# Kernel optimization log

Hardware: AMD Instinct MI355X
Metric: run time of the kernel (lower is better)

Reference implementation:

```python
import jax, jax.numpy as jnp
import numpy as np

EMB_DIM = 256
ATT_DIM = 256
B, S = 8, 2048


def setup_inputs() -> dict:
    key = jax.random.key(0)
    ks = jax.random.split(key, 9)
    scale = 1.0 / np.sqrt(EMB_DIM)
    inp = {
        "x": jax.random.normal(ks[0], (B, S, EMB_DIM), dtype=jnp.float32),
        "mask": jax.random.randint(ks[1], (B, S, S), 0, 2, dtype=jnp.int32),
        "Wq": jax.random.uniform(ks[2], (EMB_DIM, ATT_DIM), jnp.float32, -scale, scale),
        "bq": jax.random.uniform(ks[3], (ATT_DIM,), jnp.float32, -scale, scale),
        "Wk": jax.random.uniform(ks[4], (EMB_DIM, ATT_DIM), jnp.float32, -scale, scale),
        "bk": jax.random.uniform(ks[5], (ATT_DIM,), jnp.float32, -scale, scale),
        "Wv": jax.random.uniform(ks[6], (EMB_DIM, ATT_DIM), jnp.float32, -scale, scale),
        "bv": jax.random.uniform(ks[7], (ATT_DIM,), jnp.float32, -scale, scale),
    }
    return inp


def reference(x, mask, Wq, bq, Wk, bk, Wv, bv):
    # Linear projections: (B,S,E) @ (E,A) + (A,)
    q = jnp.einsum("bse,ea->bsa", x, Wq) + bq
    k = jnp.einsum("bse,ea->bsa", x, Wk) + bk
    v = jnp.einsum("bse,ea->bsa", x, Wv) + bv
    # scores: (B,S,S)
    scores = jnp.einsum("bqa,bka->bqk", q, k) / jnp.sqrt(jnp.float32(ATT_DIM))
    scores = jnp.where(mask == 0, jnp.float32(-1e9), scores)
    attn = jax.nn.softmax(scores, axis=-1)
    return jnp.einsum("bqk,bka->bqa", attn, v)
```

## Files before the change

### kernel.cpp

```cpp
#include <hip/hip_runtime.h>
#include <hip/hip_bf16.h>
#include <stdint.h>

#define BATCH 8
#define SEQ   2048
#define EMB   256
#define ADIM  256

typedef __bf16 bf16_t;
typedef __attribute__((ext_vector_type(8))) __bf16 bf16x8;
typedef __attribute__((ext_vector_type(4))) float  f32x4;
typedef uint32_t u32;
typedef __attribute__((ext_vector_type(4))) u32 u32x4;
typedef long long i64;

static __device__ __forceinline__ f32x4 mfma16(bf16x8 a, bf16x8 b, f32x4 c) {
    return __builtin_amdgcn_mfma_f32_16x16x32_bf16(a, b, c, 0, 0, 0);
}

static __device__ __forceinline__ void gld16(const void* g, void* l) {
    __builtin_amdgcn_global_load_lds((const __attribute__((address_space(1))) u32*)g,
                                     (__attribute__((address_space(3))) u32*)l, 16, 0, 0);
}

__global__ __launch_bounds__(256) void wtkv_kernel(const float* __restrict__ Wk,
                                                   const float* __restrict__ Wv,
                                                   bf16_t* __restrict__ wt) {
    int tid = blockIdx.x * 256 + threadIdx.x;
    int m = tid >> 16;
    int i = tid & 65535;
    int a = i >> 8, e = i & 255;
    const float* W = (m == 0) ? Wk : Wv;
    wt[m * 65536 + a * 256 + e] = (bf16_t)W[e * 256 + a];
}

__global__ __launch_bounds__(256) void maskbits_kernel(const u32* __restrict__ mask,
                                                       u32* __restrict__ bitw) {
    int idx = blockIdx.x * 256 + threadIdx.x;
    const u32* mp = mask + (size_t)idx * 32;
    u32 wd = 0;
    #pragma unroll
    for (int q = 0; q < 8; ++q) {
        u32x4 v = *(const u32x4*)(mp + q * 4);
        #pragma unroll
        for (int j = 0; j < 4; ++j)
            wd |= (v[j] ? 1u : 0u) << (q * 4 + j);
    }
    bitw[idx] = wd;
}

__global__ __launch_bounds__(128, 1) void proj_kv(const float* __restrict__ x,
                                                  const bf16_t* __restrict__ wt,
                                                  const float* __restrict__ bk,
                                                  const float* __restrict__ bv,
                                                  char* __restrict__ Ksw,
                                                  char* __restrict__ Vsw) {
    __shared__ __align__(16) char stg[2][10240];
    const int tid  = threadIdx.x;
    const int wid  = tid >> 6;
    const int lane = tid & 63;
    const int lq   = lane >> 4;
    const int ln   = lane & 15;
    const int blk  = blockIdx.x;
    const int b    = blk >> 6;
    const int tile = blk & 63;
    const int mbase = blk * 32 + wid * 16;
    char* S = stg[wid];

    bf16x8 xf[8];
    const float* xp = x + (size_t)(mbase + ln) * EMB;
    #pragma unroll
    for (int c = 0; c < 8; ++c) {
        f32x4 a0 = *(const f32x4*)(xp + c * 32 + lq * 8);
        f32x4 a1 = *(const f32x4*)(xp + c * 32 + lq * 8 + 4);
        bf16x8 v;
        v[0] = (bf16_t)a0[0]; v[1] = (bf16_t)a0[1]; v[2] = (bf16_t)a0[2]; v[3] = (bf16_t)a0[3];
        v[4] = (bf16_t)a1[0]; v[5] = (bf16_t)a1[1]; v[6] = (bf16_t)a1[2]; v[7] = (bf16_t)a1[3];
        xf[c] = v;
    }

    f32x4 acc[16];

    #pragma unroll
    for (int t = 0; t < 16; ++t) acc[t] = (f32x4){0.f, 0.f, 0.f, 0.f};
    {
        const bf16_t* w = wt;
        #pragma unroll
        for (int c = 0; c < 8; ++c)
            #pragma unroll
            for (int t = 0; t < 16; ++t) {
                bf16x8 wf = *(const bf16x8*)(w + (size_t)(t * 16 + ln) * 256 + c * 32 + lq * 8);
                acc[t] = mfma16(xf[c], wf, acc[t]);
            }
    }
    #pragma unroll
    for (int t = 0; t < 16; ++t) {
        float bb = bk[t * 16 + ln];
        #pragma unroll
        for (int r = 0; r < 4; ++r)
            *(bf16_t*)(S + (lq * 4 + r) * 512 + (t * 16 + ln) * 2) = (bf16_t)(acc[t][r] + bb);
    }
    asm volatile("s_waitcnt lgkmcnt(0)" ::: "memory");
    {
        char* Kg = Ksw + (size_t)b * 1048576 + (size_t)tile * 16384 + wid * 8192;
        const int rh = lane >> 5;
        const int p  = lane & 31;
        #pragma unroll
        for (int i = 0; i < 8; ++i) {
            int row = i * 2 + rh;
            int n   = wid * 16 + row;
            int cb  = p ^ (n & 7);
            f32x4 ch = *(const f32x4*)(S + row * 512 + cb * 16);
            *(f32x4*)(Kg + row * 512 + p * 16) = ch;
        }
    }

    #pragma unroll
    for (int t = 0; t < 16; ++t) acc[t] = (f32x4){0.f, 0.f, 0.f, 0.f};
    {
        const bf16_t* w = wt + 65536;
        #pragma unroll
        for (int c = 0; c < 8; ++c)
            #pragma unroll
            for (int t = 0; t < 16; ++t) {
                bf16x8 wf = *(const bf16x8*)(w + (size_t)(t * 16 + ln) * 256 + c * 32 + lq * 8);
                acc[t] = mfma16(xf[c], wf, acc[t]);
            }
    }
    #pragma unroll
    for (int t = 0; t < 16; ++t) {
        float bb = bv[t * 16 + ln];
        #pragma unroll
        for (int r = 0; r < 4; ++r)
            *(bf16_t*)(S + (t * 16 + ln) * 40 + (lq * 4 + r) * 2) = (bf16_t)(acc[t][r] + bb);
    }
    asm volatile("s_waitcnt lgkmcnt(0)" ::: "memory");
    {
        char* Vg = Vsw + (size_t)b * 1048576 + (size_t)tile * 16384;
        const int half = lane & 1;
        const int kq   = wid * 2 + half;
        #pragma unroll
        for (int i = 0; i < 8; ++i) {
            int a   = i * 32 + (lane >> 1);
            int pos = kq ^ (a & 3) ^ ((a >> 2) & 3);
            f32x4 ch = *(const f32x4*)(S + a * 40 + half * 16);
            *(f32x4*)(Vg + a * 64 + pos * 16) = ch;
        }
    }
}

__global__ __launch_bounds__(512, 4) void flash_kernel(const float* __restrict__ x,
                                                       const float* __restrict__ WqM,
                                                       const float* __restrict__ bq,
                                                       const char* __restrict__ Ksw,
                                                       const char* __restrict__ Vsw,
                                                       const int* __restrict__ mask,
                                                       const u32* __restrict__ bitw,
                                                       float* __restrict__ lp,
                                                       i64 bs, i64 rs, i64 ks,
                                                       float* __restrict__ out) {
    __shared__ __align__(16) char smem[76288];
    const int tid  = threadIdx.x;
    const int wid  = tid >> 6;
    const int lane = tid & 63;
    const int lq   = lane >> 4;
    const int ln   = lane & 15;
    const int qw   = wid >> 1;
    const int kw   = wid & 1;
    const int batch = blockIdx.x & 7;
    const int kvh   = (blockIdx.x >> 3) & 1;
    const int qbase = (blockIdx.x >> 4) * 64;

    const char* Kb = Ksw + (size_t)batch * 1048576 + (size_t)(kvh * 32) * 16384;
    const char* Vb = Vsw + (size_t)batch * 1048576 + (size_t)(kvh * 32) * 16384;
    char*  Pq_ = smem + 65536 + qw * 1280;
    char*  Pt  = smem + 65536 + wid * 1280;
    float* Ls  = (float*)(smem + 75776);

    const int dhalf = wid >> 2, dqr = wid & 3;
    const char* gsrc0 = (dhalf ? Vb : Kb) + dqr * 4096 + lane * 16;
    const int   ldst0 = dhalf * 16384 + dqr * 4096;

    const int* mroot = mask + (size_t)batch * SEQ * SEQ +
                       (size_t)(qbase + qw * 16) * SEQ + kvh * 1024 + kw * 16 + ln;
    const u32* broot = bitw ? bitw + (size_t)batch * 131072 +
                              (size_t)(qbase + qw * 16) * 64 + kvh * 32
                            : nullptr;
    const int bitpos = kw * 16 + ln;

    {
        char* dl = smem + ldst0;
        #pragma unroll
        for (int i = 0; i < 4; ++i) gld16(gsrc0 + i * 1024, dl + i * 1024);
    }
    asm volatile("" ::: "memory");
    int mv[2][4];
    if (broot) {
        #pragma unroll
        for (int w = 0; w < 2; ++w)
            #pragma unroll
            for (int r = 0; r < 4; ++r)
                mv[w][r] = (int)((broot[(lq * 4 + r) * 64 + w] >> bitpos) & 1u);
    } else {
        #pragma unroll
        for (int w = 0; w < 2; ++w)
            #pragma unroll
            for (int r = 0; r < 4; ++r)
                mv[w][r] = mroot[(size_t)(lq * 4 + r) * SEQ + w * 32];
    }

    bf16x8 qf[8];
    {
        bf16x8 xf[8];
        {
            const float* xp = x + (size_t)(batch * SEQ + qbase + qw * 16 + ln) * EMB;
            #pragma unroll
            for (int c = 0; c < 8; ++c) {
                f32x4 a = *(const f32x4*)(xp + c * 32 + lq * 8);
                f32x4 b = *(const f32x4*)(xp + c * 32 + lq * 8 + 4);
                bf16x8 v;
                v[0] = (bf16_t)a[0]; v[1] = (bf16_t)a[1]; v[2] = (bf16_t)a[2]; v[3] = (bf16_t)a[3];
                v[4] = (bf16_t)b[0]; v[5] = (bf16_t)b[1]; v[6] = (bf16_t)b[2]; v[7] = (bf16_t)b[3];
                xf[c] = v;
            }
        }
        f32x4 qacc[16];
        #pragma unroll
        for (int t = 0; t < 16; ++t) qacc[t] = (f32x4){0.f, 0.f, 0.f, 0.f};

        char* Wsp = smem + 32768;
        const int grp = tid >> 8;
        const int aa  = tid & 255;
        const int e   = ln & 7;
        #pragma unroll 1
        for (int cp = 0; cp < 8; ++cp) {
            __syncthreads();
            const float* wqp = WqM + (size_t)(cp * 32) * 256 + aa;
            #pragma unroll
            for (int i = 0; i < 2; ++i) {
                int ip = grp * 2 + i;
                bf16x8 pk;
                #pragma unroll
                for (int j = 0; j < 8; ++j)
                    pk[j] = (bf16_t)wqp[(size_t)(ip * 8 + j) * 256];
                *(bf16x8*)(Wsp + aa * 128 + ((ip ^ (aa & 7)) * 16)) = pk;
            }
            __syncthreads();
            #pragma unroll
            for (int t = 0; t < 16; ++t) {
                bf16x8 wf = *(const bf16x8*)(Wsp + (t * 16 + ln) * 128 + ((lq ^ e) * 16));
                qacc[t] = mfma16(xf[cp], wf, qacc[t]);
            }
        }
        #pragma unroll
        for (int c = 0; c < 8; ++c) {
            #pragma unroll
            for (int half2 = 0; half2 < 2; ++half2) {
                int t = 2 * c + half2;
                float bb = bq[t * 16 + ln];
                #pragma unroll
                for (int r = 0; r < 4; ++r) {
                    float v = (qacc[t][r] + bb) * 0.0625f;
                    ((bf16_t*)(Pt + (lq * 4 + r) * 80))[half2 * 16 + ln] = (bf16_t)v;
                }
            }
            qf[c] = *(const bf16x8*)(Pt + ln * 80 + lq * 16);
        }
    }

    f32x4 o[8];
    #pragma unroll
    for (int t = 0; t < 8; ++t) o[t] = (f32x4){0.f, 0.f, 0.f, 0.f};
    float lsum[4] = {0.f, 0.f, 0.f, 0.f};

    const int kswz = ln & 7;
    const int vswz = (lq ^ (ln & 3) ^ ((ln >> 2) & 3)) * 16;
    const int n0   = kw * 16 + ln;

    for (int kt = 0; kt < 32; ++kt) {
        asm volatile("s_waitcnt vmcnt(4) lgkmcnt(0)\n\ts_barrier" ::: "memory");
        if (kt + 1 < 32) {
            const char* gs = gsrc0 + (size_t)(kt + 1) * 16384;
            char* dl = smem + ((kt + 1) & 1) * 32768 + ldst0;
            #pragma unroll
            for (int i = 0; i < 4; ++i) gld16(gs + i * 1024, dl + i * 1024);
        }
        const char* Ksb = smem + (kt & 1) * 32768;
        const char* Vsb = Ksb + 16384;

        f32x4 s0 = (f32x4){0.f, 0.f, 0.f, 0.f};
        const char* krow = Ksb + n0 * 512;
        #pragma unroll
        for (int c = 0; c < 8; ++c) {
            bf16x8 kf = *(const bf16x8*)(krow + (((c * 4 + lq) ^ kswz) * 16));
            s0 = mfma16(qf[c], kf, s0);
        }

        const int* mc = mv[kt & 1];
        #pragma unroll
        for (int r = 0; r < 4; ++r) {
            float p0 = mc[r] ? __expf(s0[r]) : 0.f;
            lsum[r] += p0;
            ((bf16_t*)(Pq_ + (lq * 4 + r) * 80))[kw * 16 + ln] = (bf16_t)p0;
        }

        asm volatile("s_waitcnt lgkmcnt(0)\n\ts_barrier" ::: "memory");

        {
            const int ktn = (kt + 2 < 32) ? kt + 2 : 31;
            int* md = mv[kt & 1];
            if (broot) {
                #pragma unroll
                for (int r = 0; r < 4; ++r)
                    md[r] = (int)((broot[(lq * 4 + r) * 64 + ktn] >> bitpos) & 1u);
            } else {
                #pragma unroll
                for (int r = 0; r < 4; ++r)
                    md[r] = mroot[(size_t)(lq * 4 + r) * SEQ + ktn * 32];
            }
        }

        bf16x8 pa0 = *(const bf16x8*)(Pq_ + ln * 80 + lq * 16);

        const char* vbase = Vsb + (kw * 128 + ln) * 64 + vswz;
        #pragma unroll
        for (int t = 0; t < 8; ++t) {
            bf16x8 vf = *(const bf16x8*)(vbase + t * 1024);
            o[t] = mfma16(pa0, vf, o[t]);
        }
    }

    __syncthreads();
    #pragma unroll
    for (int r = 0; r < 4; ++r) {
        float v = lsum[r];
        v += __shfl_xor(v, 1);
        v += __shfl_xor(v, 2);
        v += __shfl_xor(v, 4);
        v += __shfl_xor(v, 8);
        if (ln == 0) Ls[(qw * 2 + kw) * 16 + lq * 4 + r] = v;
        lsum[r] = v;
    }
    __syncthreads();

    if (kw == 0 && ln == 0) {
        #pragma unroll
        for (int r = 0; r < 4; ++r) {
            int row = lq * 4 + r;
            float tot = lsum[r] + Ls[(qw * 2 + 1) * 16 + row];
            lp[bs * batch + rs * (qbase + qw * 16 + row) + ks * kvh] = tot;
        }
    }

    #pragma unroll
    for (int r = 0; r < 4; ++r) {
        float* orow = out + (size_t)(batch * SEQ + qbase + qw * 16 + lq * 4 + r) * ADIM
                      + kw * 128 + ln;
        #pragma unroll
        for (int t = 0; t < 8; ++t)
            atomicAdd(orow + t * 16, o[t][r]);
    }
}

__global__ __launch_bounds__(256) void merge_kernel(const float* __restrict__ lp,
                                                    i64 bs, i64 rs, i64 ks,
                                                    float* __restrict__ out) {
    int idx  = blockIdx.x * 256 + threadIdx.x;
    int base = idx * 4;
    int row  = base >> 8;
    int b = row >> 11, r = row & 2047;
    float l0 = lp[bs * b + rs * r];
    float l1 = lp[bs * b + rs * r + ks];
    float inv = 1.0f / (l0 + l1);
    f32x4 v = *(const f32x4*)(out + base);
    v[0] *= inv; v[1] *= inv; v[2] *= inv; v[3] *= inv;
    *(f32x4*)(out + base) = v;
}

extern "C" void kernel_launch(void* const* d_in, const int* in_sizes, int n_in,
                              void* d_out, int out_size, void* d_ws, size_t ws_size,
                              hipStream_t stream) {
    const float* x    = (const float*)d_in[0];
    int*         mask = (int*)d_in[1];
    const float* Wq   = (const float*)d_in[2];
    const float* bq   = (const float*)d_in[3];
    const float* Wk   = (const float*)d_in[4];
    const float* bk   = (const float*)d_in[5];
    const float* Wv   = (const float*)d_in[6];
    const float* bv   = (const float*)d_in[7];
    float* out = (float*)d_out;

    char* Ksw = (char*)d_ws;
    char* Vsw = Ksw + (size_t)8 * 1024 * 1024;
    bf16_t* wt = (bf16_t*)d_out;

    const size_t MB = 1024 * 1024;
    const size_t lsum_bytes = (size_t)2 * BATCH * SEQ * sizeof(float);
    u32*   bitw = nullptr;
    float* lp; i64 bs, rs, ks;
    if (ws_size >= 20 * MB + lsum_bytes) {
        bitw = (u32*)(Ksw + 16 * MB);
        lp = (float*)(Ksw + 20 * MB);
        bs = (i64)2 * SEQ;  rs = 2;  ks = 1;
    } else if (ws_size >= 16 * MB + lsum_bytes) {
        lp = (float*)(Ksw + 16 * MB);
        bs = (i64)2 * SEQ;  rs = 2;  ks = 1;
    } else {
        lp = (float*)mask;
        bs = (i64)SEQ * SEQ;  rs = SEQ;  ks = 1024;
    }

    wtkv_kernel<<<512, 256, 0, stream>>>(Wk, Wv, wt);
    if (bitw) maskbits_kernel<<<4096, 256, 0, stream>>>((const u32*)mask, bitw);
    proj_kv<<<512, 128, 0, stream>>>(x, wt, bk, bv, Ksw, Vsw);
    hipMemsetAsync(d_out, 0, (size_t)out_size * sizeof(float), stream);
    flash_kernel<<<512, 512, 0, stream>>>(x, Wq, bq, Ksw, Vsw, mask, bitw,
                                          lp, bs, rs, ks, out);
    merge_kernel<<<4096, 256, 0, stream>>>(lp, bs, rs, ks, out);
}
```

Before: 379.5 us.

## Precompute Q projection in projection kernel and simplify flash kernel to 4 waves

Moves the Q projection (with the 1/sqrt(d) scale folded in) out of the flash kernel and into the shared projection kernel, which writes a swizzled bf16 Q buffer to workspace. A new lean flash kernel with 256 threads loads Q fragments from that buffer, double-buffers K/V tiles through LDS, and feeds the bitmask straight into the exp and P-shuffle path. The previous flash kernel is kept as a fallback for when the workspace is too small. The trade is an extra 8MB workspace write and read in exchange for removing the in-kernel fp32 Q projection and reducing LDS and thread count per block. It also assumes a larger workspace is available, and it does not subtract a running max before the exponent, so it depends on scores staying small enough not to overflow.

```diff
diff --git a/kernel.cpp b/kernel.cpp
--- a/kernel.cpp
+++ b/kernel.cpp
@@ -23,14 +23,21 @@
                                      (__attribute__((address_space(3))) u32*)l, 16, 0, 0);
 }
 
+static __device__ __forceinline__ u32 pk2(float lo, float hi) {
+    u32 a = (u32)__builtin_bit_cast(unsigned short, (bf16_t)lo);
+    u32 b = (u32)__builtin_bit_cast(unsigned short, (bf16_t)hi);
+    return a | (b << 16);
+}
+
 __global__ __launch_bounds__(256) void wtkv_kernel(const float* __restrict__ Wk,
                                                    const float* __restrict__ Wv,
+                                                   const float* __restrict__ Wq,
                                                    bf16_t* __restrict__ wt) {
     int tid = blockIdx.x * 256 + threadIdx.x;
     int m = tid >> 16;
     int i = tid & 65535;
     int a = i >> 8, e = i & 255;
-    const float* W = (m == 0) ? Wk : Wv;
+    const float* W = (m == 0) ? Wk : (m == 1) ? Wv : Wq;
     wt[m * 65536 + a * 256 + e] = (bf16_t)W[e * 256 + a];
 }
 
@@ -49,12 +56,14 @@
     bitw[idx] = wd;
 }
 
-__global__ __launch_bounds__(128, 1) void proj_kv(const float* __restrict__ x,
-                                                  const bf16_t* __restrict__ wt,
-                                                  const float* __restrict__ bk,
-                                                  const float* __restrict__ bv,
-                                                  char* __restrict__ Ksw,
-                                                  char* __restrict__ Vsw) {
+__global__ __launch_bounds__(128, 1) void proj_qkv(const float* __restrict__ x,
+                                                   const bf16_t* __restrict__ wt,
+                                                   const float* __restrict__ bk,
+                                                   const float* __restrict__ bv,
+                                                   const float* __restrict__ bq,
+                                                   char* __restrict__ Ksw,
+                                                   char* __restrict__ Vsw,
+                                                   char* __restrict__ Qsw) {
     __shared__ __align__(16) char stg[2][10240];
     const int tid  = threadIdx.x;
     const int wid  = tid >> 6;
@@ -115,6 +124,43 @@
         }
     }
 
+    if (Qsw) {
+        #pragma unroll
+        for (int t = 0; t < 16; ++t) acc[t] = (f32x4){0.f, 0.f, 0.f, 0.f};
+        {
+            const bf16_t* w = wt + 131072;
+            #pragma unroll
+            for (int c = 0; c < 8; ++c)
+                #pragma unroll
+                for (int t = 0; t < 16; ++t) {
+                    bf16x8 wf = *(const bf16x8*)(w + (size_t)(t * 16 + ln) * 256 + c * 32 + lq * 8);
+                    acc[t] = mfma16(xf[c], wf, acc[t]);
+                }
+        }
+        #pragma unroll
+        for (int t = 0; t < 16; ++t) {
+            float bb = bq[t * 16 + ln];
+            #pragma unroll
+            for (int r = 0; r < 4; ++r)
+                *(bf16_t*)(S + (lq * 4 + r) * 512 + (t * 16 + ln) * 2) =
+                    (bf16_t)((acc[t][r] + bb) * 0.0625f);
+        }
+        asm volatile("s_waitcnt lgkmcnt(0)" ::: "memory");
+        {
+            char* Qg = Qsw + (size_t)b * 1048576 + (size_t)tile * 16384 + wid * 8192;
+            const int rh = lane >> 5;
+            const int p  = lane & 31;
+            #pragma unroll
+            for (int i = 0; i < 8; ++i) {
+                int row = i * 2 + rh;
+                int n   = wid * 16 + row;
+                int cb  = p ^ (n & 7);
+                f32x4 ch = *(const f32x4*)(S + row * 512 + cb * 16);
+                *(f32x4*)(Qg + row * 512 + p * 16) = ch;
+            }
+        }
+    }
+
     #pragma unroll
     for (int t = 0; t < 16; ++t) acc[t] = (f32x4){0.f, 0.f, 0.f, 0.f};
     {
@@ -149,16 +195,151 @@
     }
 }
 
-__global__ __launch_bounds__(512, 4) void flash_kernel(const float* __restrict__ x,
-                                                       const float* __restrict__ WqM,
-                                                       const float* __restrict__ bq,
+__global__ __launch_bounds__(256, 2) void flash_kernel(const char* __restrict__ Qsw,
                                                        const char* __restrict__ Ksw,
                                                        const char* __restrict__ Vsw,
-                                                       const int* __restrict__ mask,
                                                        const u32* __restrict__ bitw,
                                                        float* __restrict__ lp,
                                                        i64 bs, i64 rs, i64 ks,
                                                        float* __restrict__ out) {
+    __shared__ __align__(16) char smem[65536];
+    const int tid  = threadIdx.x;
+    const int wid  = tid >> 6;
+    const int lane = tid & 63;
+    const int lq   = lane >> 4;
+    const int ln   = lane & 15;
+    const int batch = blockIdx.x & 7;
+    const int kvh   = (blockIdx.x >> 3) & 1;
+    const int qbase = (blockIdx.x >> 4) * 64;
+
+    const char* Kb = Ksw + (size_t)batch * 1048576 + (size_t)(kvh * 32) * 16384;
+    const char* Vb = Vsw + (size_t)batch * 1048576 + (size_t)(kvh * 32) * 16384;
+
+    const char* gsrc0 = ((wid & 2) ? Vb : Kb) + (wid & 1) * 8192 + lane * 16;
+    const int   ldst0 = (wid & 2) * 8192 + (wid & 1) * 8192;
+
+    #pragma unroll
+    for (int i = 0; i < 8; ++i) gld16(gsrc0 + i * 1024, smem + ldst0 + i * 1024);
+    asm volatile("" ::: "memory");
+
+    const u32* broot = bitw + (size_t)batch * 131072 +
+                       (size_t)(qbase + wid * 16 + ln) * 64 + kvh * 32;
+    u32 mwv[2];
+    mwv[0] = broot[0];
+    mwv[1] = broot[1];
+
+    bf16x8 qf[8];
+    {
+        const int qr = qbase + wid * 16 + ln;
+        const char* qp = Qsw + (size_t)batch * 1048576 +
+                         (size_t)(qr >> 5) * 16384 + (size_t)(qr & 31) * 512;
+        const int qswz = ln & 7;
+        #pragma unroll
+        for (int c = 0; c < 8; ++c)
+            qf[c] = *(const bf16x8*)(qp + (((c * 4 + lq) ^ qswz) * 16));
+    }
+
+    f32x4 o[16];
+    #pragma unroll
+    for (int t = 0; t < 16; ++t) o[t] = (f32x4){0.f, 0.f, 0.f, 0.f};
+    float lsum = 0.f;
+
+    const int kswz = ln & 7;
+    const int vswz = (lq ^ (ln & 3) ^ ((ln >> 2) & 3)) * 16;
+    const int lq4  = lq * 4;
+    const int iA   = (((lq & 1) * 2) * 16 + ln) * 4;
+    const int iB   = iA + 64;
+    const bool lqhi = (lq & 2) != 0;
+
+    for (int kt = 0; kt < 32; ++kt) {
+        asm volatile("s_waitcnt vmcnt(1) lgkmcnt(0)\n\ts_barrier" ::: "memory");
+        if (kt + 1 < 32) {
+            const char* gs = gsrc0 + (size_t)(kt + 1) * 16384;
+            char* dl = smem + ((kt + 1) & 1) * 32768 + ldst0;
+            #pragma unroll
+            for (int i = 0; i < 8; ++i) gld16(gs + i * 1024, dl + i * 1024);
+        }
+        const char* Ksb = smem + (kt & 1) * 32768;
+        const char* Vsb = Ksb + 16384;
+
+        f32x4 sa = (f32x4){0.f, 0.f, 0.f, 0.f};
+        f32x4 sb = (f32x4){0.f, 0.f, 0.f, 0.f};
+        const char* krowa = Ksb + ln * 512;
+        const char* krowb = Ksb + (16 + ln) * 512;
+        #pragma unroll
+        for (int c = 0; c < 8; ++c) {
+            const int off = ((c * 4 + lq) ^ kswz) * 16;
+            bf16x8 ka = *(const bf16x8*)(krowa + off);
+            bf16x8 kb = *(const bf16x8*)(krowb + off);
+            sa = mfma16(ka, qf[c], sa);
+            sb = mfma16(kb, qf[c], sb);
+        }
+
+        const u32 w = mwv[kt & 1];
+        float p[8];
+        #pragma unroll
+        for (int r = 0; r < 4; ++r) {
+            p[r]     = ((w >> (lq4 + r)) & 1u)      ? __expf(sa[r]) : 0.f;
+            p[4 + r] = ((w >> (16 + lq4 + r)) & 1u) ? __expf(sb[r]) : 0.f;
+        }
+        #pragma unroll
+        for (int r = 0; r < 8; ++r) lsum += p[r];
+
+        asm volatile("" ::: "memory");
+        {
+            const int ktn = (kt + 2 < 32) ? kt + 2 : 31;
+            mwv[kt & 1] = broot[ktn];
+        }
+
+        u32 w0a = pk2(p[0], p[1]), w1a = pk2(p[2], p[3]);
+        u32 w0b = pk2(p[4], p[5]), w1b = pk2(p[6], p[7]);
+        int r0 = __builtin_amdgcn_ds_bpermute(iA, (int)w0a);
+        int r1 = __builtin_amdgcn_ds_bpermute(iA, (int)w1a);
+        int r2 = __builtin_amdgcn_ds_bpermute(iB, (int)w0a);
+        int r3 = __builtin_amdgcn_ds_bpermute(iB, (int)w1a);
+        int r4 = __builtin_amdgcn_ds_bpermute(iA, (int)w0b);
+        int r5 = __builtin_amdgcn_ds_bpermute(iA, (int)w1b);
+        int r6 = __builtin_amdgcn_ds_bpermute(iB, (int)w0b);
+        int r7 = __builtin_amdgcn_ds_bpermute(iB, (int)w1b);
+        u32x4 wv;
+        wv[0] = lqhi ? (u32)r4 : (u32)r0;
+        wv[1] = lqhi ? (u32)r5 : (u32)r1;
+        wv[2] = lqhi ? (u32)r6 : (u32)r2;
+        wv[3] = lqhi ? (u32)r7 : (u32)r3;
+        bf16x8 pa = __builtin_bit_cast(bf16x8, wv);
+
+        const char* vbase = Vsb + ln * 64 + vswz;
+        #pragma unroll
+        for (int t = 0; t < 16; ++t) {
+            bf16x8 vf = *(const bf16x8*)(vbase + t * 1024);
+            o[t] = mfma16(pa, vf, o[t]);
+        }
+    }
+
+    lsum += __shfl_xor(lsum, 16);
+    lsum += __shfl_xor(lsum, 32);
+    if (lane < 16)
+        lp[bs * batch + rs * (qbase + wid * 16 + ln) + ks * kvh] = lsum;
+
+    #pragma unroll
+    for (int r = 0; r < 4; ++r) {
+        float* orow = out + (size_t)(batch * SEQ + qbase + wid * 16 + lq4 + r) * ADIM + ln;
+        #pragma unroll
+        for (int t = 0; t < 16; ++t)
+            atomicAdd(orow + t * 16, o[t][r]);
+    }
+}
+
+__global__ __launch_bounds__(512, 4) void flash_fb(const float* __restrict__ x,
+                                                   const float* __restrict__ WqM,
+                                                   const float* __restrict__ bq,
+                                                   const char* __restrict__ Ksw,
+                                                   const char* __restrict__ Vsw,
+                                                   const int* __restrict__ mask,
+                                                   const u32* __restrict__ bitw,
+                                                   float* __restrict__ lp,
+                                                   i64 bs, i64 rs, i64 ks,
+                                                   float* __restrict__ out) {
     __shared__ __align__(16) char smem[76288];
     const int tid  = threadIdx.x;
     const int wid  = tid >> 6;
@@ -397,10 +578,16 @@
     const size_t MB = 1024 * 1024;
     const size_t lsum_bytes = (size_t)2 * BATCH * SEQ * sizeof(float);
     u32*   bitw = nullptr;
+    char*  Qsw  = nullptr;
     float* lp; i64 bs, rs, ks;
-    if (ws_size >= 20 * MB + lsum_bytes) {
+    if (ws_size >= 28 * MB + lsum_bytes) {
         bitw = (u32*)(Ksw + 16 * MB);
-        lp = (float*)(Ksw + 20 * MB);
+        Qsw  = Ksw + 20 * MB;
+        lp   = (float*)(Ksw + 28 * MB);
+        bs = (i64)2 * SEQ;  rs = 2;  ks = 1;
+    } else if (ws_size >= 20 * MB + lsum_bytes) {
+        bitw = (u32*)(Ksw + 16 * MB);
+        lp   = (float*)(Ksw + 20 * MB);
         bs = (i64)2 * SEQ;  rs = 2;  ks = 1;
     } else if (ws_size >= 16 * MB + lsum_bytes) {
         lp = (float*)(Ksw + 16 * MB);
@@ -410,11 +597,14 @@
         bs = (i64)SEQ * SEQ;  rs = SEQ;  ks = 1024;
     }
 
-    wtkv_kernel<<<512, 256, 0, stream>>>(Wk, Wv, wt);
+    wtkv_kernel<<<768, 256, 0, stream>>>(Wk, Wv, Wq, wt);
     if (bitw) maskbits_kernel<<<4096, 256, 0, stream>>>((const u32*)mask, bitw);
-    proj_kv<<<512, 128, 0, stream>>>(x, wt, bk, bv, Ksw, Vsw);
+    proj_qkv<<<512, 128, 0, stream>>>(x, wt, bk, bv, bq, Ksw, Vsw, Qsw);
     hipMemsetAsync(d_out, 0, (size_t)out_size * sizeof(float), stream);
-    flash_kernel<<<512, 512, 0, stream>>>(x, Wq, bq, Ksw, Vsw, mask, bitw,
+    if (Qsw)
+        flash_kernel<<<512, 256, 0, stream>>>(Qsw, Ksw, Vsw, bitw, lp, bs, rs, ks, out);
+    else
+        flash_fb<<<512, 512, 0, stream>>>(x, Wq, bq, Ksw, Vsw, mask, bitw,
                                           lp, bs, rs, ks, out);
     merge_kernel<<<4096, 256, 0, stream>>>(lp, bs, rs, ks, out);
 }
```

Result: faster. 359.8 us (-5.2%).
